# Kernel optimization log

Hardware: AMD Instinct MI355X
Metric: run time of the kernel (lower is better)

The kernel has to match this reference:

```python
import math
import jax, jax.numpy as jnp
import numpy as np

SCALES = (128.0, 256.0, 512.0)
ASPECT_RATIOS = (0.5, 1.0, 2.0)
NMS_THR = 0.7
PRENMS_K = 6000   # rpn_test_prenms_topk (module built with training=False)
POST_K = 300      # rpn_test_topk
MIN_SIZE = 16.0
DW_CLIP = math.log(1000.0 / 16.0)


def conv2d(x, w, b, pad):
    y = jax.lax.conv_general_dilated(
        x, w, window_strides=(1, 1), padding=[(pad, pad), (pad, pad)],
        dimension_numbers=("NCHW", "OIHW", "NCHW"))
    return y + b[None, :, None, None]


def generate_anchors(im_h, im_w, grid_h, grid_w, dtype):
    stride_h = float(im_h // grid_h)
    stride_w = float(im_w // grid_w)
    ar = jnp.asarray(ASPECT_RATIOS, dtype)
    sc = jnp.asarray(SCALES, dtype)
    h_ratios = jnp.sqrt(ar)
    w_ratios = 1.0 / h_ratios
    hs = (h_ratios[:, None] * sc[None, :]).reshape(-1)   # [A]
    ws = (w_ratios[:, None] * sc[None, :]).reshape(-1)
    base = jnp.round(jnp.stack([-ws, -hs, ws, hs], axis=1) / 2.0)  # [A,4]
    xs = jnp.arange(grid_w, dtype=dtype) * stride_w
    ys = jnp.arange(grid_h, dtype=dtype) * stride_h
    sy, sx = jnp.meshgrid(ys, xs, indexing="ij")
    sx = sx.reshape(-1); sy = sy.reshape(-1)
    shift = jnp.stack([sx, sy, sx, sy], axis=1)           # [HW,4]
    return (shift[:, None, :] + base[None, :, :]).reshape(-1, 4)  # [HW*A,4]


def decode_boxes(pred, anchors):
    # pred, anchors: [N,4] -> decoded [N,4]
    w = anchors[:, 2] - anchors[:, 0]
    h = anchors[:, 3] - anchors[:, 1]
    cx = anchors[:, 0] + 0.5 * w
    cy = anchors[:, 1] + 0.5 * h
    dx, dy = pred[:, 0], pred[:, 1]
    dw = jnp.minimum(pred[:, 2], DW_CLIP)
    dh = jnp.minimum(pred[:, 3], DW_CLIP)
    px = dx * w + cx
    py = dy * h + cy
    pw = jnp.exp(dw) * w
    ph = jnp.exp(dh) * h
    return jnp.stack([px - 0.5 * pw, py - 0.5 * ph, px + 0.5 * pw, py + 0.5 * ph], axis=1)


def nms_keep(boxes, valid, thr):
    # boxes assumed sorted by descending score; sequential greedy NMS.
    N = boxes.shape[0]
    area = (boxes[:, 2] - boxes[:, 0]) * (boxes[:, 3] - boxes[:, 1])
    idx = jnp.arange(N)

    def body(i, keep):
        b = jax.lax.dynamic_slice(boxes, (i, 0), (1, 4))[0]
        x1 = jnp.maximum(b[0], boxes[:, 0])
        y1 = jnp.maximum(b[1], boxes[:, 1])
        x2 = jnp.minimum(b[2], boxes[:, 2])
        y2 = jnp.minimum(b[3], boxes[:, 3])
        inter = jnp.clip(x2 - x1, 0.0) * jnp.clip(y2 - y1, 0.0)
        iou = inter / (area[i] + area - inter)
        suppress = (iou > thr) & (idx > i) & keep[i]
        return keep & ~suppress

    return jax.lax.fori_loop(0, N, body, valid)


def rpn_forward(image, feat, rpn_conv_w, rpn_conv_b, cls_w, cls_b, bbox_w, bbox_b):
    rpn_feat = jax.nn.relu(conv2d(feat, rpn_conv_w, rpn_conv_b, pad=1))
    cls_scores = conv2d(rpn_feat, cls_w, cls_b, pad=0)       # [B,A,H,W]
    box_pred = conv2d(rpn_feat, bbox_w, bbox_b, pad=0)       # [B,4A,H,W]
    B, A, H, W = cls_scores.shape
    im_h, im_w = image.shape[-2], image.shape[-1]
    anchors = generate_anchors(im_h, im_w, H, W, feat.dtype)  # [HWA,4]

    cls_flat = jnp.transpose(cls_scores, (0, 2, 3, 1)).reshape(-1)              # [B*H*W*A]
    pred = jnp.transpose(box_pred.reshape(B, A, 4, H, W), (0, 3, 4, 1, 2)).reshape(-1, 4)
    proposals = decode_boxes(pred, anchors)                   # [N,4]

    scores = jax.nn.sigmoid(cls_flat)
    top_scores, top_idx = jax.lax.top_k(scores, PRENMS_K)
    props = proposals[top_idx]                                # [K,4]
    # clamp to image boundary
    props = jnp.stack([
        jnp.clip(props[:, 0], 0.0, float(im_w)),
        jnp.clip(props[:, 1], 0.0, float(im_h)),
        jnp.clip(props[:, 2], 0.0, float(im_w)),
        jnp.clip(props[:, 3], 0.0, float(im_h))], axis=1)
    w = props[:, 2] - props[:, 0]
    h = props[:, 3] - props[:, 1]
    valid = (w >= MIN_SIZE) & (h >= MIN_SIZE)
    keep = nms_keep(props, valid, NMS_THR)                    # already score-sorted
    masked = jnp.where(keep, top_scores, -jnp.inf)
    final_scores, sel = jax.lax.top_k(masked, POST_K)
    final_boxes = props[sel]
    ok = jnp.isfinite(final_scores)
    final_boxes = jnp.where(ok[:, None], final_boxes, 0.0)
    final_scores = jnp.where(ok, final_scores, 0.0)
    return jnp.concatenate([final_boxes, final_scores[:, None]], axis=1)  # [POST_K,5]


def setup_inputs() -> dict:
    key = jax.random.key(0)
    ks = jax.random.split(key, 6)
    C, H, W, A = 256, 128, 128, 9
    IMH = IMW = 1024
    std = 0.01
    return {
        "image": jax.random.normal(ks[0], (1, 3, IMH, IMW), jnp.float32),
        "feat": jax.random.normal(ks[1], (1, C, H, W), jnp.float32),
        "rpn_conv_w": jax.random.normal(ks[2], (C, C, 3, 3), jnp.float32) * std,
        "rpn_conv_b": jnp.zeros((C,), jnp.float32),
        "cls_w": jax.random.normal(ks[3], (A, C, 1, 1), jnp.float32) * std,
        "cls_b": jnp.zeros((A,), jnp.float32),
        "bbox_w": jax.random.normal(ks[4], (4 * A, C, 1, 1), jnp.float32) * std,
        "bbox_b": jnp.zeros((4 * A,), jnp.float32),
    }


def reference(image, feat, rpn_conv_w, rpn_conv_b, cls_w, cls_b, bbox_w, bbox_b):
    return rpn_forward(image, feat, rpn_conv_w, rpn_conv_b, cls_w, cls_b, bbox_w, bbox_b)
```

## Files before the change

### kernel.cpp

```cpp
#include <hip/hip_runtime.h>

#define HW 128
#define NPIX 16384
#define CIN 256
#define NSC 147456
#define PRENMS 6000
#define POSTK 300
#define DW_CLIP_F 4.135166556742356f
#define MW 96
typedef unsigned long long ull;

__global__ void zero_kernel(unsigned* __restrict__ p, int n) {
    int i = blockIdx.x * 256 + threadIdx.x;
    if (i < n) p[i] = 0u;
}

__global__ void wt_kernel(const float* __restrict__ w, float* __restrict__ wt) {
    int i = blockIdx.x * 256 + threadIdx.x;
    if (i < 2304 * 256) {
        int k = i >> 8, co = i & 255;
        wt[i] = w[co * 2304 + k];
    }
}

__global__ __launch_bounds__(256) void conv3x3_half_kernel(
    const float* __restrict__ feat, const float* __restrict__ wt,
    float* __restrict__ part)
{
    __shared__ float in_s[16 * 324];
    const int tx = threadIdx.x;
    const int ty = threadIdx.y;
    const int x0 = blockIdx.x * 16;
    const int y0 = blockIdx.y * 16;
    const int h  = blockIdx.z >> 4;
    const int co0 = (blockIdx.z & 15) << 4;
    const int tid = ty * 16 + tx;

    const int yy1 = tid / 18, xx1 = tid - yy1 * 18;
    const int t2 = tid + 256;
    const int yy2 = t2 / 18, xx2 = t2 - yy2 * 18;
    const int gy1 = y0 + yy1 - 1, gx1 = x0 + xx1 - 1;
    const int gy2 = y0 + yy2 - 1, gx2 = x0 + xx2 - 1;
    const bool p1 = ((unsigned)gy1 < 128u) && ((unsigned)gx1 < 128u);
    const bool p2 = (tid < 68) && ((unsigned)gy2 < 128u) && ((unsigned)gx2 < 128u);
    const int a1 = p1 ? (gy1 * 128 + gx1) : 0;
    const int a2 = p2 ? (gy2 * 128 + gx2) : 0;

    float acc[16];
#pragma unroll
    for (int i = 0; i < 16; ++i) acc[i] = 0.f;

    const float* fh = feat + h * 128 * NPIX;
    const float* wh = wt + h * 128 * 9 * 256;

    for (int s = 0; s < 8; ++s) {
        __syncthreads();
        const float* fbase = fh + s * 16 * NPIX;
#pragma unroll
        for (int ci = 0; ci < 16; ++ci) {
            float t = fbase[ci * NPIX + a1];
            in_s[ci * 324 + tid] = p1 ? t : 0.f;
        }
        if (tid < 68) {
#pragma unroll
            for (int ci = 0; ci < 16; ++ci) {
                float t = fbase[ci * NPIX + a2];
                in_s[ci * 324 + 256 + tid] = p2 ? t : 0.f;
            }
        }
        __syncthreads();
        const float* ws0 = wh + s * 16 * 9 * 256 + co0;
#pragma unroll 4
        for (int ci = 0; ci < 16; ++ci) {
            const float* wrow = ws0 + ci * 9 * 256;
#pragma unroll
            for (int t = 0; t < 9; ++t) {
                const int ky = t / 3, kx = t - ky * 3;
                float v = in_s[ci * 324 + (ty + ky) * 18 + (tx + kx)];
                const float* wp = wrow + t * 256;
#pragma unroll
                for (int co = 0; co < 16; ++co)
                    acc[co] = fmaf(v, wp[co], acc[co]);
            }
        }
    }
    float* po = part + h * (CIN * NPIX) + co0 * NPIX + (y0 + ty) * 128 + (x0 + tx);
#pragma unroll
    for (int co = 0; co < 16; ++co)
        po[co * NPIX] = acc[co];
}

__global__ __launch_bounds__(256) void combine_kernel(
    float* __restrict__ part, const float* __restrict__ b)
{
    const int i = blockIdx.x * 256 + threadIdx.x;
    float4 a = ((const float4*)part)[i];
    float4 c = ((const float4*)(part + CIN * NPIX))[i];
    float bias = b[i >> 12];
    float4 r;
    r.x = fmaxf(a.x + c.x + bias, 0.f);
    r.y = fmaxf(a.y + c.y + bias, 0.f);
    r.z = fmaxf(a.z + c.z + bias, 0.f);
    r.w = fmaxf(a.w + c.w + bias, 0.f);
    ((float4*)part)[i] = r;
}

__global__ __launch_bounds__(64) void heads_kernel(
    const float* __restrict__ rf,
    const float* __restrict__ cls_w, const float* __restrict__ cls_b,
    const float* __restrict__ bbox_w, const float* __restrict__ bbox_b,
    float* __restrict__ scores, float* __restrict__ bb)
{
    __shared__ float wl[256][48];
    const int tid = threadIdx.x;
    for (int e = tid; e < 256 * 45; e += 64) {
        int ci = e / 45, s = e - ci * 45;
        wl[ci][s] = (s < 9) ? cls_w[s * CIN + ci] : bbox_w[(s - 9) * CIN + ci];
    }
    __syncthreads();

    const int p = blockIdx.x * 64 + tid;
    float acc[45];
#pragma unroll
    for (int i = 0; i < 45; ++i) acc[i] = 0.f;

#pragma unroll 2
    for (int ci = 0; ci < CIN; ++ci) {
        float v = rf[ci * NPIX + p];
        const float4* wr = (const float4*)&wl[ci][0];
#pragma unroll
        for (int q = 0; q < 11; ++q) {
            float4 w4 = wr[q];
            acc[q * 4 + 0] = fmaf(v, w4.x, acc[q * 4 + 0]);
            acc[q * 4 + 1] = fmaf(v, w4.y, acc[q * 4 + 1]);
            acc[q * 4 + 2] = fmaf(v, w4.z, acc[q * 4 + 2]);
            acc[q * 4 + 3] = fmaf(v, w4.w, acc[q * 4 + 3]);
        }
        acc[44] = fmaf(v, wl[ci][44], acc[44]);
    }
#pragma unroll
    for (int a = 0; a < 9; ++a) {
        float s = acc[a] + cls_b[a];
        scores[p * 9 + a] = 1.0f / (1.0f + expf(-s));
    }
#pragma unroll
    for (int c = 0; c < 36; ++c) {
        bb[c * NPIX + p] = acc[9 + c] + bbox_b[c];
    }
}

__global__ __launch_bounds__(1024) void hist1_kernel(const float* __restrict__ scores,
                                                     unsigned* __restrict__ hist1) {
    __shared__ unsigned h[16384];
    const int tid = threadIdx.x;
    for (int i = tid; i < 16384; i += 1024) h[i] = 0u;
    __syncthreads();
    for (int i = blockIdx.x * 1024 + tid; i < NSC; i += gridDim.x * 1024) {
        unsigned bits = __float_as_uint(scores[i]);
        atomicAdd(&h[bits >> 16], 1u);
    }
    __syncthreads();
    for (int i = tid; i < 16384; i += 1024) {
        unsigned c = h[i];
        if (c) atomicAdd(&hist1[i], c);
    }
}

__global__ __launch_bounds__(1024) void scan1_kernel(const unsigned* __restrict__ hist,
                                                     unsigned* __restrict__ meta) {
    __shared__ unsigned ssum[1024];
    const int t = threadIdx.x;
    unsigned local[16];
    unsigned s = 0;
#pragma unroll
    for (int i = 0; i < 16; ++i) { local[i] = hist[t * 16 + i]; s += local[i]; }
    ssum[t] = s;
    __syncthreads();
    for (int off = 1; off < 1024; off <<= 1) {
        unsigned v = ssum[t] + ((t + off < 1024) ? ssum[t + off] : 0u);
        __syncthreads();
        ssum[t] = v;
        __syncthreads();
    }
    unsigned run = ssum[t] - s;
#pragma unroll
    for (int i = 15; i >= 0; --i) {
        unsigned nb = run + local[i];
        if (nb >= (unsigned)PRENMS && run < (unsigned)PRENMS) {
            meta[1] = (unsigned)(t * 16 + i);
            meta[2] = run;
        }
        run = nb;
    }
}

__global__ void hist2_kernel(const float* __restrict__ scores, const unsigned* __restrict__ meta,
                             unsigned* __restrict__ hist2) {
    int i = blockIdx.x * 256 + threadIdx.x;
    if (i < NSC) {
        unsigned bits = __float_as_uint(scores[i]);
        if ((bits >> 16) == meta[1]) atomicAdd(&hist2[bits & 0xFFFFu], 1u);
    }
}

__global__ __launch_bounds__(1024) void scan2_kernel(const unsigned* __restrict__ hist2,
                                                     unsigned* __restrict__ meta) {
    __shared__ unsigned ssum[1024];
    const int t = threadIdx.x;
    const unsigned need = (unsigned)PRENMS - meta[2];
    unsigned s = 0;
    for (int i = 0; i < 64; ++i) s += hist2[t * 64 + i];
    ssum[t] = s;
    __syncthreads();
    for (int off = 1; off < 1024; off <<= 1) {
        unsigned v = ssum[t] + ((t + off < 1024) ? ssum[t + off] : 0u);
        __syncthreads();
        ssum[t] = v;
        __syncthreads();
    }
    unsigned run = ssum[t] - s;
    for (int i = 63; i >= 0; --i) {
        unsigned h = hist2[t * 64 + i];
        unsigned nb = run + h;
        if (nb >= need && run < need) {
            meta[3] = (meta[1] << 16) | (unsigned)(t * 64 + i);
        }
        run = nb;
    }
}

__global__ void compact_kernel(const float* __restrict__ scores, unsigned* __restrict__ meta,
                               ull* __restrict__ cand) {
    int i = blockIdx.x * 256 + threadIdx.x;
    unsigned bits = (i < NSC) ? __float_as_uint(scores[i]) : 0u;
    bool pred = (i < NSC) && (bits >= meta[3]);
    ull bal = __ballot(pred);
    int lane = threadIdx.x & 63;
    unsigned cnt = (unsigned)__popcll(bal);
    unsigned base = 0;
    if (lane == 0 && cnt) base = atomicAdd(&meta[0], cnt);
    base = __shfl(base, 0);
    if (pred) {
        unsigned off = (unsigned)__popcll(bal & ((1ull << lane) - 1ull));
        unsigned pos = base + off;
        if (pos < 8192u)
            cand[pos] = ((ull)bits << 32) | (unsigned)(~i);
    }
}

__global__ __launch_bounds__(1024) void sortA_kernel(const ull* __restrict__ cand,
                                                     const unsigned* __restrict__ meta,
                                                     ull* __restrict__ sorted) {
    __shared__ ull keys[2048];
    const int tid = threadIdx.x;
    const int base = blockIdx.x * 2048;
    const int n = min((int)meta[0], 8192);
    for (int i = tid; i < 2048; i += 1024) {
        int g = base + i;
        keys[i] = (g < n) ? cand[g] : (ull)(8191 - g);
    }
    __syncthreads();
    for (int k = 2; k <= 2048; k <<= 1) {
        for (int j = k >> 1; j >= 1; j >>= 1) {
            int s = tid;
            int i = ((s & ~(j - 1)) << 1) | (s & (j - 1));
            int p = i | j;
            ull a = keys[i], c = keys[p];
            bool desc = ((i & k) == 0);
            bool sw = desc ? (a < c) : (a > c);
            if (sw) { keys[i] = c; keys[p] = a; }
            __syncthreads();
        }
    }
    for (int i = tid; i < 2048; i += 1024) sorted[base + i] = keys[i];
}

__global__ __launch_bounds__(256) void merge_kernel(const ull* __restrict__ sorted,
                                                    ull* __restrict__ fin) {
    const int g = blockIdx.x * 256 + threadIdx.x;
    ull x = sorted[g];
    const int c = g >> 11;
    int rank = g & 2047;
#pragma unroll
    for (int cc = 0; cc < 4; ++cc) {
        if (cc == c) continue;
        const ull* arr = sorted + cc * 2048;
        int lo = 0, hi = 2048;
        while (lo < hi) { int mid = (lo + hi) >> 1; if (arr[mid] > x) lo = mid + 1; else hi = mid; }
        rank += lo;
    }
    fin[rank] = x;
}

__global__ __launch_bounds__(64) void decode_kernel(
    const ull* __restrict__ fin, const float* __restrict__ bb,
    float* __restrict__ selbox, float* __restrict__ selsc,
    ull* __restrict__ validbits)
{
    const int r = blockIdx.x * 64 + threadIdx.x;
    int valid = 0;
    if (r < PRENMS) {
        ull key = fin[r];
        unsigned sbits = (unsigned)(key >> 32);
        unsigned idx = ~(unsigned)(key & 0xFFFFFFFFull);
        float score = __uint_as_float(sbits);
        int p = (int)(idx / 9u);
        int a = (int)(idx - (unsigned)p * 9u);
        int y = p >> 7, x = p & 127;
        float d0 = bb[(a * 4 + 0) * NPIX + p];
        float d1 = bb[(a * 4 + 1) * NPIX + p];
        float d2 = bb[(a * 4 + 2) * NPIX + p];
        float d3 = bb[(a * 4 + 3) * NPIX + p];
        int ar_i = a / 3, sc_i = a - ar_i * 3;
        float arv = (ar_i == 0) ? 0.5f : ((ar_i == 1) ? 1.0f : 2.0f);
        float scv = (sc_i == 0) ? 128.f : ((sc_i == 1) ? 256.f : 512.f);
        float hr = sqrtf(arv);
        float wr = 1.0f / hr;
        float hs = hr * scv;
        float wsv = wr * scv;
        float bx1 = rintf(-wsv * 0.5f), by1 = rintf(-hs * 0.5f);
        float bx2 = rintf(wsv * 0.5f),  by2 = rintf(hs * 0.5f);
        float ax1 = x * 8.f + bx1, ay1 = y * 8.f + by1;
        float ax2 = x * 8.f + bx2, ay2 = y * 8.f + by2;
        float wa = ax2 - ax1, ha = ay2 - ay1;
        float cx = ax1 + 0.5f * wa, cy = ay1 + 0.5f * ha;
        float dw = fminf(d2, DW_CLIP_F), dh = fminf(d3, DW_CLIP_F);
        float px = d0 * wa + cx, py = d1 * ha + cy;
        float pw = expf(dw) * wa, ph = expf(dh) * ha;
        float x1 = px - 0.5f * pw, y1 = py - 0.5f * ph;
        float x2 = px + 0.5f * pw, y2 = py + 0.5f * ph;
        x1 = fminf(fmaxf(x1, 0.f), 1024.f);
        y1 = fminf(fmaxf(y1, 0.f), 1024.f);
        x2 = fminf(fmaxf(x2, 0.f), 1024.f);
        y2 = fminf(fmaxf(y2, 0.f), 1024.f);
        float bw = x2 - x1, bh = y2 - y1;
        valid = (bw >= 16.f) && (bh >= 16.f);
        selbox[r * 4 + 0] = x1; selbox[r * 4 + 1] = y1;
        selbox[r * 4 + 2] = x2; selbox[r * 4 + 3] = y2;
        selsc[r] = score;
    }
    ull bal = __ballot(valid);
    if (threadIdx.x == 0) validbits[blockIdx.x] = bal;
}

__global__ __launch_bounds__(256) void maskbuild_kernel(
    const float* __restrict__ selbox, ull* __restrict__ mask)
{
    __shared__ float jb0[64], jb1[64], jb2[64], jb3[64];
    const int jw = blockIdx.y;
    const int tid = threadIdx.x;
    const int i = blockIdx.x * 256 + tid;
    if (jw * 64 + 63 < blockIdx.x * 256) {
        if (i < PRENMS) mask[(size_t)i * MW + jw] = 0ull;
        return;
    }
    if (tid < 64) {
        int j = jw * 64 + tid;
        float x1 = 0.f, y1 = 0.f, x2 = 0.f, y2 = 0.f;
        if (j < PRENMS) {
            x1 = selbox[j * 4 + 0]; y1 = selbox[j * 4 + 1];
            x2 = selbox[j * 4 + 2]; y2 = selbox[j * 4 + 3];
        }
        jb0[tid] = x1; jb1[tid] = y1; jb2[tid] = x2; jb3[tid] = y2;
    }
    __syncthreads();
    if (i >= PRENMS) return;
    const float ix1 = selbox[i * 4 + 0], iy1 = selbox[i * 4 + 1];
    const float ix2 = selbox[i * 4 + 2], iy2 = selbox[i * 4 + 3];
    const float iarea = (ix2 - ix1) * (iy2 - iy1);
    ull word = 0ull;
    for (int b = 0; b < 64; ++b) {
        int j = jw * 64 + b;
        float xx1 = fmaxf(ix1, jb0[b]);
        float yy1 = fmaxf(iy1, jb1[b]);
        float xx2 = fminf(ix2, jb2[b]);
        float yy2 = fminf(iy2, jb3[b]);
        float iw = fmaxf(xx2 - xx1, 0.f);
        float ih = fmaxf(yy2 - yy1, 0.f);
        float inter = iw * ih;
        float jarea = (jb2[b] - jb0[b]) * (jb3[b] - jb1[b]);
        float iou = inter / (iarea + jarea - inter);
        if (j > i && iou > 0.7f) word |= (1ull << b);
    }
    mask[(size_t)i * MW + jw] = word;
}

__global__ __launch_bounds__(64) void nms_scan_kernel(
    const ull* __restrict__ validbits,
    const ull* __restrict__ mask,
    const float* __restrict__ selbox, const float* __restrict__ selsc,
    float* __restrict__ out)
{
    __shared__ int kept[POSTK];
    const int l = threadIdx.x;
    ull supp0 = ~validbits[l];
    ull supp1 = (l < 30) ? ~validbits[64 + l] : ~0ull;
    int nk = 0;
    ull ownrow_next = mask[(size_t)l * MW + 0];
    for (int wi = 0; wi < 94 && nk < POSTK; ++wi) {
        ull ownrow = ownrow_next;
        if (wi < 93) ownrow_next = mask[(size_t)((wi + 1) * 64 + l) * MW + (wi + 1)];
        ull wsup = (wi < 64) ? __shfl(supp0, wi) : __shfl(supp1, wi - 64);
        ull active = ~wsup;
        if (!active) continue;
        ull keptbits = 0ull;
        while (active && nk < POSTK) {
            int b = __builtin_ctzll(active);
            keptbits |= (1ull << b);
            if (l == 0) kept[nk] = wi * 64 + b;
            nk++;
            ull rowb = __shfl(ownrow, b);
            ull gt = (b == 63) ? 0ull : (~0ull << (b + 1));
            active &= gt & ~rowb;
        }
        while (keptbits) {
            int b0 = __builtin_ctzll(keptbits); keptbits &= keptbits - 1;
            int b1 = -1, b2 = -1, b3 = -1;
            if (keptbits) { b1 = __builtin_ctzll(keptbits); keptbits &= keptbits - 1; }
            if (keptbits) { b2 = __builtin_ctzll(keptbits); keptbits &= keptbits - 1; }
            if (keptbits) { b3 = __builtin_ctzll(keptbits); keptbits &= keptbits - 1; }
            const ull* r0 = mask + (size_t)(wi * 64 + b0) * MW;
            ull t0a = r0[l], t0b = (l < 30) ? r0[64 + l] : 0ull;
            ull t1a = 0, t1b = 0, t2a = 0, t2b = 0, t3a = 0, t3b = 0;
            if (b1 >= 0) { const ull* r1 = mask + (size_t)(wi * 64 + b1) * MW; t1a = r1[l]; t1b = (l < 30) ? r1[64 + l] : 0ull; }
            if (b2 >= 0) { const ull* r2 = mask + (size_t)(wi * 64 + b2) * MW; t2a = r2[l]; t2b = (l < 30) ? r2[64 + l] : 0ull; }
            if (b3 >= 0) { const ull* r3 = mask + (size_t)(wi * 64 + b3) * MW; t3a = r3[l]; t3b = (l < 30) ? r3[64 + l] : 0ull; }
            supp0 |= t0a | t1a | t2a | t3a;
            supp1 |= t0b | t1b | t2b | t3b;
        }
    }
    __syncthreads();
    for (int r = l; r < POSTK; r += 64) {
        if (r < nk) {
            int i = kept[r];
            out[r * 5 + 0] = selbox[i * 4 + 0];
            out[r * 5 + 1] = selbox[i * 4 + 1];
            out[r * 5 + 2] = selbox[i * 4 + 2];
            out[r * 5 + 3] = selbox[i * 4 + 3];
            out[r * 5 + 4] = selsc[i];
        } else {
            out[r * 5 + 0] = 0.f; out[r * 5 + 1] = 0.f;
            out[r * 5 + 2] = 0.f; out[r * 5 + 3] = 0.f;
            out[r * 5 + 4] = 0.f;
        }
    }
}

extern "C" void kernel_launch(void* const* d_in, const int* in_sizes, int n_in,
                              void* d_out, int out_size, void* d_ws, size_t ws_size,
                              hipStream_t stream) {
    const float* feat    = (const float*)d_in[1];
    const float* conv_w  = (const float*)d_in[2];
    const float* conv_b  = (const float*)d_in[3];
    const float* cls_w   = (const float*)d_in[4];
    const float* cls_b   = (const float*)d_in[5];
    const float* bbox_w  = (const float*)d_in[6];
    const float* bbox_b  = (const float*)d_in[7];
    float* out = (float*)d_out;

    char* ws = (char*)d_ws;
    float*    part      = (float*)(ws + 0);
    float*    rpn_feat  = part;
    float*    wt        = (float*)(ws + 33554432);
    float*    bb        = (float*)(ws + 35913728);
    float*    scores    = (float*)(ws + 38273024);
    unsigned* hist1     = (unsigned*)(ws + 38862848);
    unsigned* hist2     = (unsigned*)(ws + 38928384);
    unsigned* meta      = (unsigned*)(ws + 39190528);
    ull*      cand      = (ull*)(ws + 39190784);
    ull*      sorted    = (ull*)(ws + 39256320);
    ull*      fin       = (ull*)(ws + 39321856);
    float*    selbox    = (float*)(ws + 39387392);
    float*    selsc     = (float*)(ws + 39483648);
    ull*      validbits = (ull*)(ws + 39507712);
    ull*      mask      = (ull*)(ws + 39508480);

    {
        int nz = 16384 + 65536 + 64;
        zero_kernel<<<(nz + 255) / 256, 256, 0, stream>>>(hist1, nz);
    }
    wt_kernel<<<(2304 * 256 + 255) / 256, 256, 0, stream>>>(conv_w, wt);
    conv3x3_half_kernel<<<dim3(8, 8, 32), dim3(16, 16), 0, stream>>>(feat, wt, part);
    combine_kernel<<<4096, 256, 0, stream>>>(part, conv_b);
    heads_kernel<<<256, 64, 0, stream>>>(rpn_feat, cls_w, cls_b, bbox_w, bbox_b, scores, bb);
    hist1_kernel<<<64, 1024, 0, stream>>>(scores, hist1);
    scan1_kernel<<<1, 1024, 0, stream>>>(hist1, meta);
    hist2_kernel<<<(NSC + 255) / 256, 256, 0, stream>>>(scores, meta, hist2);
    scan2_kernel<<<1, 1024, 0, stream>>>(hist2, meta);
    compact_kernel<<<(NSC + 255) / 256, 256, 0, stream>>>(scores, meta, cand);
    sortA_kernel<<<4, 1024, 0, stream>>>(cand, meta, sorted);
    merge_kernel<<<32, 256, 0, stream>>>(sorted, fin);
    decode_kernel<<<94, 64, 0, stream>>>(fin, bb, selbox, selsc, validbits);
    maskbuild_kernel<<<dim3(24, 94), 256, 0, stream>>>(selbox, mask);
    nms_scan_kernel<<<1, 64, 0, stream>>>(validbits, mask, selbox, selsc, out);
}
```

Baseline: 584.6 us.

## Fuse split-K combine into heads, merge prep kernels, halve conv smem stage

Removes the separate combine kernel: the heads kernel now sums the two conv partial halves, adds bias and applies ReLU while reading, with a 4-deep register prefetch of the partial values. It also merges the zeroing and weight-transpose kernels into one launch, and halves the conv shared-memory staging chunk from 16 to 8 input channels, which doubles the number of sync stages. The intent is to save a full read-modify-write pass over the 32 MB partial buffer and two launches. In exchange, heads now reads twice as much data with only 256 small blocks, so that kernel may become slower, and the conv does more barrier round trips.

```diff
diff --git a/kernel.cpp b/kernel.cpp
--- a/kernel.cpp
+++ b/kernel.cpp
@@ -10,13 +10,10 @@
 #define MW 96
 typedef unsigned long long ull;
 
-__global__ void zero_kernel(unsigned* __restrict__ p, int n) {
+__global__ void prep_kernel(const float* __restrict__ w, float* __restrict__ wt,
+                            unsigned* __restrict__ zp, int nz) {
     int i = blockIdx.x * 256 + threadIdx.x;
-    if (i < n) p[i] = 0u;
-}
-
-__global__ void wt_kernel(const float* __restrict__ w, float* __restrict__ wt) {
-    int i = blockIdx.x * 256 + threadIdx.x;
+    if (i < nz) zp[i] = 0u;
     if (i < 2304 * 256) {
         int k = i >> 8, co = i & 255;
         wt[i] = w[co * 2304 + k];
@@ -27,7 +24,7 @@
     const float* __restrict__ feat, const float* __restrict__ wt,
     float* __restrict__ part)
 {
-    __shared__ float in_s[16 * 324];
+    __shared__ float in_s[8 * 324];
     const int tx = threadIdx.x;
     const int ty = threadIdx.y;
     const int x0 = blockIdx.x * 16;
@@ -53,25 +50,25 @@
     const float* fh = feat + h * 128 * NPIX;
     const float* wh = wt + h * 128 * 9 * 256;
 
-    for (int s = 0; s < 8; ++s) {
-        __syncthreads();
-        const float* fbase = fh + s * 16 * NPIX;
-#pragma unroll
-        for (int ci = 0; ci < 16; ++ci) {
+    for (int s = 0; s < 16; ++s) {
+        __syncthreads();
+        const float* fbase = fh + s * 8 * NPIX;
+#pragma unroll
+        for (int ci = 0; ci < 8; ++ci) {
             float t = fbase[ci * NPIX + a1];
             in_s[ci * 324 + tid] = p1 ? t : 0.f;
         }
         if (tid < 68) {
 #pragma unroll
-            for (int ci = 0; ci < 16; ++ci) {
+            for (int ci = 0; ci < 8; ++ci) {
                 float t = fbase[ci * NPIX + a2];
                 in_s[ci * 324 + 256 + tid] = p2 ? t : 0.f;
             }
         }
         __syncthreads();
-        const float* ws0 = wh + s * 16 * 9 * 256 + co0;
+        const float* ws0 = wh + s * 8 * 9 * 256 + co0;
 #pragma unroll 4
-        for (int ci = 0; ci < 16; ++ci) {
+        for (int ci = 0; ci < 8; ++ci) {
             const float* wrow = ws0 + ci * 9 * 256;
 #pragma unroll
             for (int t = 0; t < 9; ++t) {
@@ -90,23 +87,8 @@
         po[co * NPIX] = acc[co];
 }
 
-__global__ __launch_bounds__(256) void combine_kernel(
-    float* __restrict__ part, const float* __restrict__ b)
-{
-    const int i = blockIdx.x * 256 + threadIdx.x;
-    float4 a = ((const float4*)part)[i];
-    float4 c = ((const float4*)(part + CIN * NPIX))[i];
-    float bias = b[i >> 12];
-    float4 r;
-    r.x = fmaxf(a.x + c.x + bias, 0.f);
-    r.y = fmaxf(a.y + c.y + bias, 0.f);
-    r.z = fmaxf(a.z + c.z + bias, 0.f);
-    r.w = fmaxf(a.w + c.w + bias, 0.f);
-    ((float4*)part)[i] = r;
-}
-
 __global__ __launch_bounds__(64) void heads_kernel(
-    const float* __restrict__ rf,
+    const float* __restrict__ part, const float* __restrict__ conv_b,
     const float* __restrict__ cls_w, const float* __restrict__ cls_b,
     const float* __restrict__ bbox_w, const float* __restrict__ bbox_b,
     float* __restrict__ scores, float* __restrict__ bb)
@@ -114,19 +96,29 @@
     __shared__ float wl[256][48];
     const int tid = threadIdx.x;
     for (int e = tid; e < 256 * 45; e += 64) {
-        int ci = e / 45, s = e - ci * 45;
+        int s = e >> 8, ci = e & 255;
         wl[ci][s] = (s < 9) ? cls_w[s * CIN + ci] : bbox_w[(s - 9) * CIN + ci];
     }
     __syncthreads();
 
     const int p = blockIdx.x * 64 + tid;
+    const float* p0 = part + p;
+    const float* p1s = part + CIN * NPIX + p;
     float acc[45];
 #pragma unroll
     for (int i = 0; i < 45; ++i) acc[i] = 0.f;
 
-#pragma unroll 2
+    float va[4], vb[4];
+#pragma unroll
+    for (int k = 0; k < 4; ++k) { va[k] = p0[k * NPIX]; vb[k] = p1s[k * NPIX]; }
+
+#pragma unroll 4
     for (int ci = 0; ci < CIN; ++ci) {
-        float v = rf[ci * NPIX + p];
+        float v = fmaxf(va[ci & 3] + vb[ci & 3] + conv_b[ci], 0.f);
+        if (ci + 4 < CIN) {
+            va[ci & 3] = p0[(ci + 4) * NPIX];
+            vb[ci & 3] = p1s[(ci + 4) * NPIX];
+        }
         const float4* wr = (const float4*)&wl[ci][0];
 #pragma unroll
         for (int q = 0; q < 11; ++q) {
@@ -460,7 +452,6 @@
 
     char* ws = (char*)d_ws;
     float*    part      = (float*)(ws + 0);
-    float*    rpn_feat  = part;
     float*    wt        = (float*)(ws + 33554432);
     float*    bb        = (float*)(ws + 35913728);
     float*    scores    = (float*)(ws + 38273024);
@@ -471,18 +462,14 @@
     ull*      sorted    = (ull*)(ws + 39256320);
     ull*      fin       = (ull*)(ws + 39321856);
     float*    selbox    = (float*)(ws + 39387392);
-    float*    selsc     = (float*)(ws + 39483648);
+    float*    selsc    = (float*)(ws + 39483648);
     ull*      validbits = (ull*)(ws + 39507712);
     ull*      mask      = (ull*)(ws + 39508480);
 
-    {
-        int nz = 16384 + 65536 + 64;
-        zero_kernel<<<(nz + 255) / 256, 256, 0, stream>>>(hist1, nz);
-    }
-    wt_kernel<<<(2304 * 256 + 255) / 256, 256, 0, stream>>>(conv_w, wt);
+    const int nz = 16384 + 65536 + 64;
+    prep_kernel<<<(2304 * 256 + 255) / 256, 256, 0, stream>>>(conv_w, wt, hist1, nz);
     conv3x3_half_kernel<<<dim3(8, 8, 32), dim3(16, 16), 0, stream>>>(feat, wt, part);
-    combine_kernel<<<4096, 256, 0, stream>>>(part, conv_b);
-    heads_kernel<<<256, 64, 0, stream>>>(rpn_feat, cls_w, cls_b, bbox_w, bbox_b, scores, bb);
+    heads_kernel<<<256, 64, 0, stream>>>(part, conv_b, cls_w, cls_b, bbox_w, bbox_b, scores, bb);
     hist1_kernel<<<64, 1024, 0, stream>>>(scores, hist1);
     scan1_kernel<<<1, 1024, 0, stream>>>(hist1, meta);
     hist2_kernel<<<(NSC + 255) / 256, 256, 0, stream>>>(scores, meta, hist2);
```

New measurement: 629.8 us. 1.08x slower.
